# Optimization experiments

Hardware: AMD Instinct MI355X
Metric: run time of the kernel (lower is better)

## Reference

```python
import jax, jax.numpy as jnp
import numpy as np

NUM_PB, PB = 32, 16
D, H, L = 64, 1024, 2
B, T = 64, 256


def setup_inputs() -> dict:
    key = jax.random.key(0)
    ks = jax.random.split(key, 16)
    s = 0.02
    return {
        "sequence_label": jax.random.randint(ks[0], (B,), 0, NUM_PB),
        "forward_computation_length": T,
        "mu_pb": jax.random.normal(ks[1], (NUM_PB, PB), jnp.float32),
        "logvar_pb": jax.random.normal(ks[2], (NUM_PB, PB), jnp.float32),
        "W_ih0": jax.random.normal(ks[3], (4 * H, D + PB), jnp.float32) * s,
        "W_hh0": jax.random.normal(ks[4], (4 * H, H), jnp.float32) * s,
        "b_ih0": jax.random.normal(ks[5], (4 * H,), jnp.float32) * s,
        "b_hh0": jax.random.normal(ks[6], (4 * H,), jnp.float32) * s,
        "W_ih1": jax.random.normal(ks[7], (4 * H, H), jnp.float32) * s,
        "W_hh1": jax.random.normal(ks[8], (4 * H, H), jnp.float32) * s,
        "b_ih1": jax.random.normal(ks[9], (4 * H,), jnp.float32) * s,
        "b_hh1": jax.random.normal(ks[10], (4 * H,), jnp.float32) * s,
        "W_lin": jax.random.normal(ks[11], (D, H), jnp.float32) * s,
        "b_lin": jax.random.normal(ks[12], (D,), jnp.float32) * s,
    }


def _lstm_cell(x, h, c, Wi, Wh, bi, bh):
    # PyTorch gate order: i, f, g, o
    g = x @ Wi.T + bi + h @ Wh.T + bh  # [B, 4H]
    i_, f_, g_, o_ = jnp.split(g, 4, axis=-1)
    c_new = jax.nn.sigmoid(f_) * c + jax.nn.sigmoid(i_) * jnp.tanh(g_)
    h_new = jax.nn.sigmoid(o_) * jnp.tanh(c_new)
    return h_new, c_new


def reference(sequence_label, forward_computation_length, mu_pb, logvar_pb,
              W_ih0, W_hh0, b_ih0, b_hh0, W_ih1, W_hh1, b_ih1, b_hh1,
              W_lin, b_lin):
    b = sequence_label.shape[0]
    mu_sel = mu_pb[sequence_label]        # [B, PB]
    logvar_sel = logvar_pb[sequence_label]
    pb = mu_sel                            # deterministic behavior
    dt = mu_pb.dtype
    h0 = jnp.zeros((L, b, H), dt)
    c0 = jnp.zeros((L, b, H), dt)
    y0 = jnp.zeros((b, D), dt)
    layers = ((W_ih0, W_hh0, b_ih0, b_hh0), (W_ih1, W_hh1, b_ih1, b_hh1))

    def step(carry, _):
        h, c, prev = carry
        inp = jnp.concatenate([prev, pb], axis=-1)  # [B, D+PB]
        hs, cs = [], []
        for l, (Wi, Wh, bi, bh) in enumerate(layers):
            hl, cl = _lstm_cell(inp, h[l], c[l], Wi, Wh, bi, bh)
            hs.append(hl)
            cs.append(cl)
            inp = hl
        out = inp @ W_lin.T + b_lin  # [B, D]
        return (jnp.stack(hs), jnp.stack(cs), out), out

    _, outputs = jax.lax.scan(step, (h0, c0, y0), None,
                              length=forward_computation_length)
    return outputs, sequence_label, pb, mu_sel, logvar_sel
```

## Files before the change

### kernel.cpp

```cpp
#include <hip/hip_runtime.h>
#include <math.h>

#define NUM_PB 32
#define PBDIM  16
#define DDIM   64
#define HDIM   1024
#define BDIM   64

typedef __attribute__((ext_vector_type(8))) short bf16x8;
typedef __attribute__((ext_vector_type(4))) float f32x4;
typedef __attribute__((ext_vector_type(4))) unsigned int u32x4;

#define WST    1032
#define SW_MAT (16 * WST)
#define SMEM_BYTES (4 * SW_MAT * 2 + 16 * 64 * 4 + 512)

#define CTR_BASE 0xAAAAAAAAu

struct Params {
    const int*   label;
    const int*   fcl;
    const float* mu_pb;
    const float* logvar_pb;
    const float* Wi0;
    const float* Wh0;
    const float* bi0;
    const float* bh0;
    const float* Wi1;
    const float* Wh1;
    const float* bi1;
    const float* bh1;
    const float* Wlin;
    const float* blin;
    float*       out;
    float*       ws;
};

__device__ __forceinline__ unsigned short f2bf(float x) {
    unsigned int u = __builtin_bit_cast(unsigned int, x);
    u += 0x7fffu + ((u >> 16) & 1u);
    return (unsigned short)(u >> 16);
}
__device__ __forceinline__ float sigf(float x)  { return 1.0f / (1.0f + __expf(-x)); }
__device__ __forceinline__ float tanh_(float x) { float e = __expf(2.0f * x); return 1.0f - 2.0f / (e + 1.0f); }

template <int K0, int K1>
__device__ __forceinline__ void mfma_regB(const unsigned short* __restrict__ Ab,
                                          const bf16x8* Bf, f32x4* accs) {
#pragma unroll
    for (int kb = K0; kb < K1; ++kb) {
        bf16x8 a = *(const bf16x8*)(Ab + kb * 32);
        accs[kb & 3] = __builtin_amdgcn_mfma_f32_16x16x32_bf16(a, Bf[kb], accs[kb & 3], 0, 0, 0);
    }
}

__device__ __forceinline__ void issue_frag_loads_alt(const unsigned short* __restrict__ base,
                                                     int lane, bf16x8* dst) {
    const unsigned short* gp = base + lane * 8;
#pragma unroll
    for (int kb = 0; kb < 32; ++kb)
        asm volatile("global_load_dwordx4 %0, %1, off sc0 sc1"
                     : "=v"(dst[kb]) : "v"(gp + kb * 512));
}
#define VMWAIT(N) do { asm volatile("s_waitcnt vmcnt(" #N ")" ::: "memory"); \
                       __builtin_amdgcn_sched_barrier(0); } while (0)

__device__ __forceinline__ void gbar_wait_fast(char* wsBase, int tid, unsigned barIdx) {
    if (tid < 64) {
        const u32x4* sp = (const u32x4*)wsBase + tid;
        unsigned tgt = CTR_BASE + barIdx;
        while (true) {
            u32x4 v;
            asm volatile("global_load_dwordx4 %0, %1, off sc0 sc1\n\t"
                         "s_waitcnt vmcnt(0)"
                         : "=v"(v) : "v"(sp) : "memory");
            int ok = (v.x >= tgt) && (v.y >= tgt) && (v.z >= tgt) && (v.w >= tgt);
            if (__all(ok)) break;
            __builtin_amdgcn_s_sleep(1);
        }
    }
    __syncthreads();
}

__device__ __forceinline__ void gbar_arrive_fast(char* wsBase, unsigned short* bufBase,
                                                 int pubOff, const unsigned short* sH,
                                                 int bid, int tid, unsigned barIdx) {
    __syncthreads();
    if (tid < 64) {
        unsigned long long v = *(const unsigned long long*)(sH + tid * 4);
        __hip_atomic_store((unsigned long long*)(bufBase + pubOff), v,
                           __ATOMIC_RELAXED, __HIP_MEMORY_SCOPE_AGENT);
    }
    if (tid == 0) {
        asm volatile("s_waitcnt vmcnt(0)" ::: "memory");
        __hip_atomic_store((unsigned*)(wsBase + (size_t)bid * 4), CTR_BASE + barIdx,
                           __ATOMIC_RELAXED, __HIP_MEMORY_SCOPE_AGENT);
    }
}

__device__ __forceinline__ void gbar_full(char* wsBase, int bid, int tid, unsigned barIdx) {
    __syncthreads();
    if (tid == 0) {
        __builtin_amdgcn_fence(__ATOMIC_RELEASE, "agent");
        __hip_atomic_store((unsigned*)(wsBase + (size_t)bid * 4), CTR_BASE + barIdx,
                           __ATOMIC_RELAXED, __HIP_MEMORY_SCOPE_AGENT);
    }
    if (tid < 64) {
        const u32x4* sp = (const u32x4*)wsBase + tid;
        unsigned tgt = CTR_BASE + barIdx;
        while (true) {
            u32x4 v;
            asm volatile("global_load_dwordx4 %0, %1, off sc0 sc1\n\t"
                         "s_waitcnt vmcnt(0)"
                         : "=v"(v) : "v"(sp) : "memory");
            int ok = (v.x >= tgt) && (v.y >= tgt) && (v.z >= tgt) && (v.w >= tgt);
            if (__all(ok)) break;
            __builtin_amdgcn_s_sleep(1);
        }
    }
    __syncthreads();
    __builtin_amdgcn_fence(__ATOMIC_ACQUIRE, "agent");
}

__global__ void __launch_bounds__(256, 1) rnn_kernel(Params p) {
    extern __shared__ __align__(16) unsigned short smem[];
    unsigned short* sWf  = smem;
    unsigned short* sWh0 = sWf + SW_MAT;
    unsigned short* sWi1 = sWh0 + SW_MAT;
    unsigned short* sWh1 = sWi1 + SW_MAT;
    float* tmpf = (float*)(smem + 4 * SW_MAT);
    unsigned short* sH = (unsigned short*)(tmpf + 16 * 64);

    const int tid = threadIdx.x, bid = blockIdx.x;
    const int lane = tid & 63, w = tid >> 6;
    const int lm = lane & 15, lq = lane >> 4;
    const int bcol0 = w * 16;
    const int bb = bcol0 + lm;
    const int j0 = bid * 4, jj = j0 + lq;
    const int T = p.fcl[0];

    unsigned short* x80g = (unsigned short*)p.ws;
    unsigned short* h0g  = x80g + 64 * 128;
    unsigned short* h1g  = h0g + 2 * 65536;
    unsigned short* wlg  = h1g + 2 * 65536;

    const int pubOff = ((tid >> 4) << 14) + ((j0 >> 5) << 9)
                     + ((((j0 >> 3) & 3) * 16 + (tid & 15)) << 3) + (j0 & 7);

    for (int idx = tid; idx < 16 * 1024; idx += 256) {
        int m = idx >> 10, k = idx & 1023;
        int gi = m & 3, jq = m >> 2;
        size_t row = (size_t)(gi * HDIM + j0 + jq);
        sWh0[m * WST + k] = f2bf(p.Wh0[row * HDIM + k]);
        sWi1[m * WST + k] = f2bf(p.Wi1[row * HDIM + k]);
        sWh1[m * WST + k] = f2bf(p.Wh1[row * HDIM + k]);
    }
    for (int i = tid; i < 16 * 64; i += 256) {
        int m = i >> 6, d = i & 63;
        int gi = m & 3, jq = m >> 2;
        tmpf[i] = p.Wi0[(size_t)(gi * HDIM + j0 + jq) * (DDIM + PBDIM) + d];
    }
    __syncthreads();
    {
        int m = tid >> 4, c = tid & 15;
        const float* wrow = tmpf + m * 64;
        for (int pass = 0; pass < 4; ++pass) {
            int k0 = c * 64 + pass * 16;
            float acc[16];
#pragma unroll
            for (int i = 0; i < 16; ++i) acc[i] = 0.f;
            for (int d = 0; d < 64; ++d) {
                float wv = wrow[d];
                const float4* wl = (const float4*)(p.Wlin + (size_t)d * HDIM + k0);
                float4 a0 = wl[0], a1 = wl[1], a2 = wl[2], a3 = wl[3];
                acc[0]  = fmaf(wv, a0.x, acc[0]);  acc[1]  = fmaf(wv, a0.y, acc[1]);
                acc[2]  = fmaf(wv, a0.z, acc[2]);  acc[3]  = fmaf(wv, a0.w, acc[3]);
                acc[4]  = fmaf(wv, a1.x, acc[4]);  acc[5]  = fmaf(wv, a1.y, acc[5]);
                acc[6]  = fmaf(wv, a1.z, acc[6]);  acc[7]  = fmaf(wv, a1.w, acc[7]);
                acc[8]  = fmaf(wv, a2.x, acc[8]);  acc[9]  = fmaf(wv, a2.y, acc[9]);
                acc[10] = fmaf(wv, a2.z, acc[10]); acc[11] = fmaf(wv, a2.w, acc[11]);
                acc[12] = fmaf(wv, a3.x, acc[12]); acc[13] = fmaf(wv, a3.y, acc[13]);
                acc[14] = fmaf(wv, a3.z, acc[14]); acc[15] = fmaf(wv, a3.w, acc[15]);
            }
#pragma unroll
            for (int i = 0; i < 16; ++i) sWf[m * WST + k0 + i] = f2bf(acc[i]);
        }
    }
    float accT0[4], yb[4], bias1[4];
    {
        int lbl = p.label[bb];
#pragma unroll
        for (int r = 0; r < 4; ++r) {
            float a0_ = p.bi0[r * HDIM + jj] + p.bh0[r * HDIM + jj];
            const float* wpb = p.Wi0 + (size_t)(r * HDIM + jj) * (DDIM + PBDIM) + DDIM;
            const float* mu  = p.mu_pb + lbl * PBDIM;
            for (int q = 0; q < PBDIM; ++q) a0_ = fmaf(wpb[q], mu[q], a0_);
            accT0[r] = a0_;
            float y_ = 0.f;
            const float* wrow = tmpf + (lq * 4 + r) * 64;
            for (int d = 0; d < 64; ++d) y_ = fmaf(wrow[d], p.blin[d], y_);
            yb[r] = y_;
            bias1[r] = p.bi1[r * HDIM + jj] + p.bh1[r * HDIM + jj];
        }
    }
    int gid = bid * 256 + tid;
    h0g[gid] = 0;
    h1g[gid] = 0;
    if (bid < 16) {
        for (int i = 0; i < 16; ++i) {
            int e = bid * 4096 + i * 256 + tid;
            wlg[e] = f2bf(p.Wlin[e]);
        }
    }
    if (bid == 16 && tid < BDIM) {
        int lbl = p.label[tid];
        float* out_lbl = p.out + (size_t)T * BDIM * DDIM;
        float* out_pb  = out_lbl + BDIM;
        float* out_mu  = out_pb + BDIM * PBDIM;
        float* out_lv  = out_mu + BDIM * PBDIM;
        out_lbl[tid] = (float)lbl;
        for (int q = 0; q < PBDIM; ++q) {
            float mu = p.mu_pb[lbl * PBDIM + q];
            float lv = p.logvar_pb[lbl * PBDIM + q];
            out_pb[tid * PBDIM + q] = mu;
            out_mu[tid * PBDIM + q] = mu;
            out_lv[tid * PBDIM + q] = lv;
        }
    }
    float blin4[4] = {0.f, 0.f, 0.f, 0.f};
    if (bid < 4) {
        int d0 = bid * 16 + lq * 4;
#pragma unroll
        for (int r = 0; r < 4; ++r) blin4[r] = p.blin[d0 + r];
    }
    float c0 = 0.f, c1 = 0.f;
    char* wsBase = (char*)p.ws;

    const f32x4 zf = {0.f, 0.f, 0.f, 0.f};
    unsigned barIdx = 1;
    gbar_full(wsBase, bid, tid, barIdx);

    f32x4 saved0 = zf;
    f32x4 saved1 = zf;
    int cur = 0;
    for (int t = 0; t < T; ++t) {
        {
            gbar_wait_fast(wsBase, tid, barIdx);
            const unsigned short* src = h1g + (size_t)cur * 65536 + (w << 14);
            bf16x8 bfrag[32];
            issue_frag_loads_alt(src, lane, bfrag);
            f32x4 accs[4] = {zf, zf, zf, zf};
            const unsigned short* Ab = sWf + lm * WST + 8 * lq;
            VMWAIT(16);
            mfma_regB<0, 16>(Ab, bfrag, accs);
            VMWAIT(0);
            mfma_regB<16, 32>(Ab, bfrag, accs);
            f32x4 s = accs[0] + accs[1] + accs[2] + accs[3];
            s += saved0;
            float addy = (t > 0) ? 1.f : 0.f;
            float gi_ = s[0] + accT0[0] + addy * yb[0];
            float gf_ = s[1] + accT0[1] + addy * yb[1];
            float gg_ = s[2] + accT0[2] + addy * yb[2];
            float go_ = s[3] + accT0[3] + addy * yb[3];
            c0 = sigf(gf_) * c0 + sigf(gi_) * tanh_(gg_);
            float h = sigf(go_) * tanh_(c0);
            sH[bb * 4 + lq] = f2bf(h);
            gbar_arrive_fast(wsBase, h0g + (size_t)(cur ^ 1) * 65536, pubOff,
                             sH, bid, tid, ++barIdx);
            if (bid < 4 && t > 0) {
                f32x4 ya[4] = {zf, zf, zf, zf};
                mfma_regB<0, 32>(wlg + (size_t)(bid * 16 + lm) * 1024 + 8 * lq, bfrag, ya);
                f32x4 sy = ya[0] + ya[1] + ya[2] + ya[3];
                int d0 = bid * 16 + lq * 4;
                float4 y4;
                y4.x = sy[0] + blin4[0]; y4.y = sy[1] + blin4[1];
                y4.z = sy[2] + blin4[2]; y4.w = sy[3] + blin4[3];
                *(float4*)(p.out + (size_t)(t - 1) * BDIM * DDIM + bb * DDIM + d0) = y4;
            }
            {
                f32x4 pa[4] = {zf, zf, zf, zf};
                mfma_regB<0, 32>(sWh1 + lm * WST + 8 * lq, bfrag, pa);
                saved1 = pa[0] + pa[1] + pa[2] + pa[3];
            }
        }
        {
            gbar_wait_fast(wsBase, tid, barIdx);
            const unsigned short* src = h0g + (size_t)(cur ^ 1) * 65536 + (w << 14);
            bf16x8 bfrag[32];
            issue_frag_loads_alt(src, lane, bfrag);
            f32x4 accs[4] = {zf, zf, zf, zf};
            const unsigned short* Ab = sWi1 + lm * WST + 8 * lq;
            VMWAIT(16);
            mfma_regB<0, 16>(Ab, bfrag, accs);
            VMWAIT(0);
            mfma_regB<16, 32>(Ab, bfrag, accs);
            f32x4 s = accs[0] + accs[1] + accs[2] + accs[3];
            s += saved1;
            float gi_ = s[0] + bias1[0], gf_ = s[1] + bias1[1];
            float gg_ = s[2] + bias1[2], go_ = s[3] + bias1[3];
            c1 = sigf(gf_) * c1 + sigf(gi_) * tanh_(gg_);
            float h = sigf(go_) * tanh_(c1);
            sH[bb * 4 + lq] = f2bf(h);
            gbar_arrive_fast(wsBase, h1g + (size_t)(cur ^ 1) * 65536, pubOff,
                             sH, bid, tid, ++barIdx);
            {
                f32x4 pa[4] = {zf, zf, zf, zf};
                mfma_regB<0, 32>(sWh0 + lm * WST + 8 * lq, bfrag, pa);
                saved0 = pa[0] + pa[1] + pa[2] + pa[3];
            }
        }
        cur ^= 1;
    }
    gbar_wait_fast(wsBase, tid, barIdx);
    if (bid < 4 && T > 0) {
        bf16x8 bfrag[32];
        issue_frag_loads_alt(h1g + (size_t)cur * 65536 + (w << 14), lane, bfrag);
        VMWAIT(0);
        f32x4 ya[4] = {zf, zf, zf, zf};
        mfma_regB<0, 32>(wlg + (size_t)(bid * 16 + lm) * 1024 + 8 * lq, bfrag, ya);
        f32x4 sy = ya[0] + ya[1] + ya[2] + ya[3];
        int d0 = bid * 16 + lq * 4;
        float4 y4;
        y4.x = sy[0] + blin4[0]; y4.y = sy[1] + blin4[1];
        y4.z = sy[2] + blin4[2]; y4.w = sy[3] + blin4[3];
        *(float4*)(p.out + (size_t)(T - 1) * BDIM * DDIM + bb * DDIM + d0) = y4;
    }
}

extern "C" void kernel_launch(void* const* d_in, const int* in_sizes, int n_in,
                              void* d_out, int out_size, void* d_ws, size_t ws_size,
                              hipStream_t stream) {
    Params p;
    p.label     = (const int*)d_in[0];
    p.fcl       = (const int*)d_in[1];
    p.mu_pb     = (const float*)d_in[2];
    p.logvar_pb = (const float*)d_in[3];
    p.Wi0       = (const float*)d_in[4];
    p.Wh0       = (const float*)d_in[5];
    p.bi0       = (const float*)d_in[6];
    p.bh0       = (const float*)d_in[7];
    p.Wi1       = (const float*)d_in[8];
    p.Wh1       = (const float*)d_in[9];
    p.bi1       = (const float*)d_in[10];
    p.bh1       = (const float*)d_in[11];
    p.Wlin      = (const float*)d_in[12];
    p.blin      = (const float*)d_in[13];
    p.out       = (float*)d_out;
    p.ws        = (float*)d_ws;

    (void)hipFuncSetAttribute((const void*)rnn_kernel,
                              hipFuncAttributeMaxDynamicSharedMemorySize, SMEM_BYTES);
    void* args[] = { &p };
    hipError_t e = hipLaunchCooperativeKernel((void*)rnn_kernel, dim3(256), dim3(256),
                                              args, SMEM_BYTES, stream);
    if (e != hipSuccess) {
        rnn_kernel<<<dim3(256), dim3(256), SMEM_BYTES, stream>>>(p);
    }
}
```

Before: 2.909 ms.

## Replace block-level grid barrier with per-wave arrival counters and polling

Each wave now publishes its own slice of the hidden state and sets its own arrival counter, and each wave polls all 1024 per-wave counters by itself. This removes the __syncthreads calls around every arrive and wait in the recurrent loop, so waves can proceed without waiting for sibling waves. The cost is four times more counters to poll per barrier, which adds memory traffic, and a dependence on each wave only needing data that has been published and matches its own batch slice.

```diff
diff --git a/kernel.cpp b/kernel.cpp
--- a/kernel.cpp
+++ b/kernel.cpp
@@ -43,6 +43,7 @@
 }
 __device__ __forceinline__ float sigf(float x)  { return 1.0f / (1.0f + __expf(-x)); }
 __device__ __forceinline__ float tanh_(float x) { float e = __expf(2.0f * x); return 1.0f - 2.0f / (e + 1.0f); }
+__device__ __forceinline__ unsigned umin_(unsigned a, unsigned b) { return a < b ? a : b; }
 
 template <int K0, int K1>
 __device__ __forceinline__ void mfma_regB(const unsigned short* __restrict__ Ab,
@@ -65,61 +66,58 @@
 #define VMWAIT(N) do { asm volatile("s_waitcnt vmcnt(" #N ")" ::: "memory"); \
                        __builtin_amdgcn_sched_barrier(0); } while (0)
 
-__device__ __forceinline__ void gbar_wait_fast(char* wsBase, int tid, unsigned barIdx) {
-    if (tid < 64) {
-        const u32x4* sp = (const u32x4*)wsBase + tid;
-        unsigned tgt = CTR_BASE + barIdx;
-        while (true) {
-            u32x4 v;
-            asm volatile("global_load_dwordx4 %0, %1, off sc0 sc1\n\t"
-                         "s_waitcnt vmcnt(0)"
-                         : "=v"(v) : "v"(sp) : "memory");
-            int ok = (v.x >= tgt) && (v.y >= tgt) && (v.z >= tgt) && (v.w >= tgt);
-            if (__all(ok)) break;
-            __builtin_amdgcn_s_sleep(1);
-        }
-    }
-    __syncthreads();
-}
-
-__device__ __forceinline__ void gbar_arrive_fast(char* wsBase, unsigned short* bufBase,
-                                                 int pubOff, const unsigned short* sH,
-                                                 int bid, int tid, unsigned barIdx) {
-    __syncthreads();
-    if (tid < 64) {
-        unsigned long long v = *(const unsigned long long*)(sH + tid * 4);
-        __hip_atomic_store((unsigned long long*)(bufBase + pubOff), v,
+__device__ __forceinline__ void poll_seq_wave(const char* wsBase, unsigned tgt) {
+    const u32x4* sp = (const u32x4*)wsBase + ((threadIdx.x & 63) << 2);
+    while (true) {
+        u32x4 v0, v1, v2, v3;
+        asm volatile("global_load_dwordx4 %0, %4, off sc0 sc1\n\t"
+                     "global_load_dwordx4 %1, %5, off sc0 sc1\n\t"
+                     "global_load_dwordx4 %2, %6, off sc0 sc1\n\t"
+                     "global_load_dwordx4 %3, %7, off sc0 sc1\n\t"
+                     "s_waitcnt vmcnt(0)"
+                     : "=v"(v0), "=v"(v1), "=v"(v2), "=v"(v3)
+                     : "v"(sp), "v"(sp + 1), "v"(sp + 2), "v"(sp + 3)
+                     : "memory");
+        unsigned m0 = umin_(umin_(v0.x, v0.y), umin_(v0.z, v0.w));
+        unsigned m1 = umin_(umin_(v1.x, v1.y), umin_(v1.z, v1.w));
+        unsigned m2 = umin_(umin_(v2.x, v2.y), umin_(v2.z, v2.w));
+        unsigned m3 = umin_(umin_(v3.x, v3.y), umin_(v3.z, v3.w));
+        unsigned mm = umin_(umin_(m0, m1), umin_(m2, m3));
+        if (__all(mm >= tgt)) break;
+        __builtin_amdgcn_s_sleep(1);
+    }
+    __builtin_amdgcn_sched_barrier(0);
+}
+
+__device__ __forceinline__ void wave_arrive(char* wsBase, unsigned short* bufBase,
+                                            const unsigned short* sHwave, int pubBase,
+                                            int seqIdx, int lane, unsigned barIdx) {
+    asm volatile("s_waitcnt lgkmcnt(0)" ::: "memory");
+    __builtin_amdgcn_sched_barrier(0);
+    if (lane < 16) {
+        unsigned long long v = *(const unsigned long long*)(sHwave + lane * 4);
+        __hip_atomic_store((unsigned long long*)(bufBase + pubBase + (lane << 3)), v,
                            __ATOMIC_RELAXED, __HIP_MEMORY_SCOPE_AGENT);
     }
-    if (tid == 0) {
-        asm volatile("s_waitcnt vmcnt(0)" ::: "memory");
-        __hip_atomic_store((unsigned*)(wsBase + (size_t)bid * 4), CTR_BASE + barIdx,
+    asm volatile("s_waitcnt vmcnt(0)" ::: "memory");
+    __builtin_amdgcn_sched_barrier(0);
+    if (lane == 0)
+        __hip_atomic_store((unsigned*)(wsBase + (size_t)seqIdx * 4), CTR_BASE + barIdx,
                            __ATOMIC_RELAXED, __HIP_MEMORY_SCOPE_AGENT);
-    }
-}
-
-__device__ __forceinline__ void gbar_full(char* wsBase, int bid, int tid, unsigned barIdx) {
-    __syncthreads();
-    if (tid == 0) {
+}
+
+__device__ __forceinline__ void gbar_full_init(char* wsBase, int bid, int w, int lane) {
+    __syncthreads();
+    if (threadIdx.x == 0)
         __builtin_amdgcn_fence(__ATOMIC_RELEASE, "agent");
-        __hip_atomic_store((unsigned*)(wsBase + (size_t)bid * 4), CTR_BASE + barIdx,
+    __syncthreads();
+    if (lane == 0)
+        __hip_atomic_store((unsigned*)(wsBase + (size_t)(bid * 4 + w) * 4), CTR_BASE + 1u,
                            __ATOMIC_RELAXED, __HIP_MEMORY_SCOPE_AGENT);
-    }
-    if (tid < 64) {
-        const u32x4* sp = (const u32x4*)wsBase + tid;
-        unsigned tgt = CTR_BASE + barIdx;
-        while (true) {
-            u32x4 v;
-            asm volatile("global_load_dwordx4 %0, %1, off sc0 sc1\n\t"
-                         "s_waitcnt vmcnt(0)"
-                         : "=v"(v) : "v"(sp) : "memory");
-            int ok = (v.x >= tgt) && (v.y >= tgt) && (v.z >= tgt) && (v.w >= tgt);
-            if (__all(ok)) break;
-            __builtin_amdgcn_s_sleep(1);
-        }
-    }
+    poll_seq_wave(wsBase, CTR_BASE + 1u);
     __syncthreads();
     __builtin_amdgcn_fence(__ATOMIC_ACQUIRE, "agent");
+    __syncthreads();
 }
 
 __global__ void __launch_bounds__(256, 1) rnn_kernel(Params p) {
@@ -129,7 +127,7 @@
     unsigned short* sWi1 = sWh0 + SW_MAT;
     unsigned short* sWh1 = sWi1 + SW_MAT;
     float* tmpf = (float*)(smem + 4 * SW_MAT);
-    unsigned short* sH = (unsigned short*)(tmpf + 16 * 64);
+    unsigned short* sHw = (unsigned short*)(tmpf + 16 * 64);
 
     const int tid = threadIdx.x, bid = blockIdx.x;
     const int lane = tid & 63, w = tid >> 6;
@@ -143,9 +141,10 @@
     unsigned short* h0g  = x80g + 64 * 128;
     unsigned short* h1g  = h0g + 2 * 65536;
     unsigned short* wlg  = h1g + 2 * 65536;
-
-    const int pubOff = ((tid >> 4) << 14) + ((j0 >> 5) << 9)
-                     + ((((j0 >> 3) & 3) * 16 + (tid & 15)) << 3) + (j0 & 7);
+    char* wsBase = (char*)p.ws;
+
+    const int pubBase = (w << 14) + ((j0 >> 5) << 9) + (((j0 >> 3) & 3) << 7) + (j0 & 7);
+    unsigned short* sHwave = sHw + w * 64;
 
     for (int idx = tid; idx < 16 * 1024; idx += 256) {
         int m = idx >> 10, k = idx & 1023;
@@ -234,18 +233,17 @@
         for (int r = 0; r < 4; ++r) blin4[r] = p.blin[d0 + r];
     }
     float c0 = 0.f, c1 = 0.f;
-    char* wsBase = (char*)p.ws;
 
     const f32x4 zf = {0.f, 0.f, 0.f, 0.f};
     unsigned barIdx = 1;
-    gbar_full(wsBase, bid, tid, barIdx);
+    gbar_full_init(wsBase, bid, w, lane);
 
     f32x4 saved0 = zf;
     f32x4 saved1 = zf;
     int cur = 0;
     for (int t = 0; t < T; ++t) {
         {
-            gbar_wait_fast(wsBase, tid, barIdx);
+            poll_seq_wave(wsBase, CTR_BASE + barIdx);
             const unsigned short* src = h1g + (size_t)cur * 65536 + (w << 14);
             bf16x8 bfrag[32];
             issue_frag_loads_alt(src, lane, bfrag);
@@ -264,9 +262,9 @@
             float go_ = s[3] + accT0[3] + addy * yb[3];
             c0 = sigf(gf_) * c0 + sigf(gi_) * tanh_(gg_);
             float h = sigf(go_) * tanh_(c0);
-            sH[bb * 4 + lq] = f2bf(h);
-            gbar_arrive_fast(wsBase, h0g + (size_t)(cur ^ 1) * 65536, pubOff,
-                             sH, bid, tid, ++barIdx);
+            sHwave[lm * 4 + lq] = f2bf(h);
+            wave_arrive(wsBase, h0g + (size_t)(cur ^ 1) * 65536, sHwave, pubBase,
+                        bid * 4 + w, lane, ++barIdx);
             if (bid < 4 && t > 0) {
                 f32x4 ya[4] = {zf, zf, zf, zf};
                 mfma_regB<0, 32>(wlg + (size_t)(bid * 16 + lm) * 1024 + 8 * lq, bfrag, ya);
@@ -284,7 +282,7 @@
             }
         }
         {
-            gbar_wait_fast(wsBase, tid, barIdx);
+            poll_seq_wave(wsBase, CTR_BASE + barIdx);
             const unsigned short* src = h0g + (size_t)(cur ^ 1) * 65536 + (w << 14);
             bf16x8 bfrag[32];
             issue_frag_loads_alt(src, lane, bfrag);
@@ -300,9 +298,9 @@
             float gg_ = s[2] + bias1[2], go_ = s[3] + bias1[3];
             c1 = sigf(gf_) * c1 + sigf(gi_) * tanh_(gg_);
             float h = sigf(go_) * tanh_(c1);
-            sH[bb * 4 + lq] = f2bf(h);
-            gbar_arrive_fast(wsBase, h1g + (size_t)(cur ^ 1) * 65536, pubOff,
-                             sH, bid, tid, ++barIdx);
+            sHwave[lm * 4 + lq] = f2bf(h);
+            wave_arrive(wsBase, h1g + (size_t)(cur ^ 1) * 65536, sHwave, pubBase,
+                        bid * 4 + w, lane, ++barIdx);
             {
                 f32x4 pa[4] = {zf, zf, zf, zf};
                 mfma_regB<0, 32>(sWh0 + lm * WST + 8 * lq, bfrag, pa);
@@ -311,8 +309,8 @@
         }
         cur ^= 1;
     }
-    gbar_wait_fast(wsBase, tid, barIdx);
     if (bid < 4 && T > 0) {
+        poll_seq_wave(wsBase, CTR_BASE + barIdx);
         bf16x8 bfrag[32];
         issue_frag_loads_alt(h1g + (size_t)cur * 65536 + (w << 14), lane, bfrag);
         VMWAIT(0);
```

New measurement: 4.369 ms. +50.2%, slower.
